# Optimization experiments

Hardware: AMD Instinct MI355X
Metric: run time of the kernel (lower is better)

Reference implementation:

```python
import jax, jax.numpy as jnp
import numpy as np

D_MODEL = 1024
D_STATE = 16
D_CONV = 4
EXPAND = 2
INNER = EXPAND * D_MODEL          # 2048
DT_RANK = max(D_MODEL // 16, 1)   # 64
B_SZ, L_SEQ = 2, 2048


def setup_inputs() -> dict:
    key = jax.random.key(0)
    ks = jax.random.split(key, 9)
    s = 0.02
    x = jax.random.normal(ks[0], (B_SZ, L_SEQ, D_MODEL), jnp.float32)
    W_in = jax.random.normal(ks[1], (2 * INNER, D_MODEL), jnp.float32) * s
    conv_w = jax.random.normal(ks[2], (INNER, 1, D_CONV), jnp.float32) * s
    conv_b = jax.random.normal(ks[3], (INNER,), jnp.float32) * s
    W_x = jax.random.normal(ks[4], (DT_RANK + 2 * D_STATE, INNER), jnp.float32) * s
    W_dt = jax.random.normal(ks[5], (INNER, DT_RANK), jnp.float32) * s
    b_dt = jax.random.normal(ks[6], (INNER,), jnp.float32) * s
    A_log = jnp.log(jnp.broadcast_to(
        jnp.arange(1, D_STATE + 1, dtype=jnp.float32), (INNER, D_STATE)))
    D_param = jnp.ones((INNER,), jnp.float32)
    W_out = jax.random.normal(ks[7], (D_MODEL, INNER), jnp.float32) * s
    return {"x": x, "W_in": W_in, "conv_w": conv_w, "conv_b": conv_b,
            "W_x": W_x, "W_dt": W_dt, "b_dt": b_dt,
            "A_log": A_log, "D_param": D_param, "W_out": W_out}


def _mamba_fwd(x, W_in, conv_w, conv_b, W_x, W_dt, b_dt, A_log, D_param, W_out):
    b, l, d = x.shape
    inner = W_in.shape[0] // 2
    dt_rank = W_dt.shape[1]
    n = A_log.shape[1]

    # in_proj and chunk
    xr = x @ W_in.T                               # [B, L, 2*inner]
    xs, res = xr[..., :inner], xr[..., inner:]

    # depthwise causal conv1d (torch pads d_conv-1 both sides then truncates to l,
    # equivalent to left-pad d_conv-1 + valid conv)
    xc = jnp.transpose(xs, (0, 2, 1))             # [B, inner, L]
    xc = jax.lax.conv_general_dilated(
        xc, conv_w, window_strides=(1,),
        padding=[(conv_w.shape[-1] - 1, 0)],
        dimension_numbers=("NCH", "OIH", "NCH"),
        feature_group_count=inner) + conv_b[None, :, None]
    xs = jax.nn.silu(jnp.transpose(xc, (0, 2, 1)))  # [B, L, inner]

    # x_proj -> dt, B, C
    x_dbl = xs @ W_x.T                            # [B, L, dt_rank + 2n]
    dt = jax.nn.softplus(x_dbl[..., :dt_rank] @ W_dt.T + b_dt)  # [B, L, inner]
    Bm = x_dbl[..., dt_rank:dt_rank + n]          # [B, L, n]
    Cm = x_dbl[..., dt_rank + n:]                 # [B, L, n]

    A = -jnp.exp(A_log)                           # [inner, n]
    # NOTE: original applies softplus a second time inside selective_scan
    dt2 = jax.nn.softplus(dt)

    def step(h, inp):
        dt_t, B_t, C_t, x_t = inp                 # [B,inner],[B,n],[B,n],[B,inner]
        dA = jnp.exp(dt_t[..., None] * A)         # [B, inner, n]
        h = dA * h + dt_t[..., None] * B_t[:, None, :] * x_t[..., None]
        y = jnp.einsum("bdn,bn->bd", h, C_t)
        return h, y

    tfirst = lambda a: jnp.swapaxes(a, 0, 1)      # [B,L,...] -> [L,B,...]
    h0 = jnp.zeros((b, inner, n), x.dtype)
    _, ys = jax.lax.scan(step, h0, (tfirst(dt2), tfirst(Bm), tfirst(Cm), tfirst(xs)))
    y = jnp.swapaxes(ys, 0, 1)                    # [B, L, inner]

    y = y + xs * D_param
    y = y * jax.nn.silu(res)
    return y @ W_out.T                            # [B, L, d_model]


def reference(x, W_in, conv_w, conv_b, W_x, W_dt, b_dt, A_log, D_param, W_out):
    return _mamba_fwd(x, W_in, conv_w, conv_b, W_x, W_dt, b_dt, A_log, D_param, W_out)
```

## Files before the change

kernel.cpp:

```cpp
#include <hip/hip_runtime.h>

#define LSEQ 2048

typedef unsigned short u16;
typedef short short8 __attribute__((ext_vector_type(8)));
typedef float f32x4 __attribute__((ext_vector_type(4)));

__device__ __forceinline__ u16 f2bf(float f) {
    unsigned u = __builtin_bit_cast(unsigned, f);
    u += 0x7fffu + ((u >> 16) & 1u);
    return (u16)(u >> 16);
}
__device__ __forceinline__ float bf2f(u16 h) {
    return __builtin_bit_cast(float, (unsigned)h << 16);
}
__device__ __forceinline__ float softplus_f(float x) {
    return fmaxf(x, 0.f) + __logf(1.f + __expf(-fabsf(x)));
}
__device__ __forceinline__ float silu_f(float x) {
    return x / (1.f + __expf(-x));
}

__device__ __forceinline__ void epowers(float e1, float* ep) {
    float e2 = e1 * e1, e4 = e2 * e2, e8 = e4 * e4;
    ep[0] = e1;       ep[1] = e2;       ep[2] = e1 * e2;  ep[3] = e4;
    ep[4] = e1 * e4;  ep[5] = e2 * e4;  ep[6] = ep[2] * e4; ep[7] = e8;
    ep[8] = e1 * e8;  ep[9] = e2 * e8;  ep[10] = ep[2] * e8; ep[11] = e4 * e8;
    ep[12] = ep[4] * e8; ep[13] = ep[5] * e8; ep[14] = ep[6] * e8; ep[15] = e8 * e8;
}

__device__ __forceinline__ void gl16(const u16* g, u16* l) {
    __builtin_amdgcn_global_load_lds(
        (const __attribute__((address_space(1))) unsigned int*)g,
        (__attribute__((address_space(3))) unsigned int*)l, 16, 0, 0);
}

#define BAR()   asm volatile("s_barrier" ::: "memory")
#define MEMFENCE() do { asm volatile("" ::: "memory"); __builtin_amdgcn_sched_barrier(0); } while (0)

template <int MODE>
__global__ __launch_bounds__(512, 2) void gemm8p(
    const u16* __restrict__ A, int lda,
    const u16* __restrict__ W, int ldw,
    float* __restrict__ C, int ldc, size_t zstride,
    int K, int n_store, u16* __restrict__ out2, u16* __restrict__ out2b)
{
    extern __shared__ u16 lds[];
    const int t    = threadIdx.x;
    const int lane = t & 63, quad = lane >> 4, lr = lane & 15;
    const int w    = t >> 6;
    const int wr   = w >> 2, wc = w & 3;

    int bm, bn;
    if (MODE == 3) {
        int lin = blockIdx.y * 16 + blockIdx.x;
        int swz = (lin & 7) * 32 + (lin >> 3);
        bm = swz >> 4; bn = swz & 15;
    } else {
        bm = blockIdx.y; bn = blockIdx.x;
    }
    const int z  = blockIdx.z;
    const int kz = z * K;

    const int srow = t >> 3;
    const int scol = (((t & 7) ^ (srow & 7)) << 3);
    const u16* pAg = A + (size_t)(bm * 256 + srow) * lda + kz + scol;
    const u16* pWg = W + (size_t)(bn * 256 + srow) * ldw + kz + scol;
    const int ldsw = w * 512;

#define STA(buf, h, i, k0) \
    gl16(pAg + (size_t)((h) * 128 + (i) * 64) * lda + (k0), \
         lds + (buf) * 32768 + (h) * 8192 + (i) * 4096 + ldsw)
#define STB(buf, h, i, k0) \
    gl16(pWg + (size_t)((h) * 128 + (i) * 64) * ldw + (k0), \
         lds + (buf) * 32768 + 16384 + (h) * 8192 + (i) * 4096 + ldsw)

    const int aBase = (wr * 128 + lr) * 64;
    const int bBase = 16384 + (wc * 64 + lr) * 64;
    const int cof0  = ((quad)     ^ (lr & 7)) << 3;
    const int cof1  = ((quad | 4) ^ (lr & 7)) << 3;

    f32x4 acc[8][4];
    #pragma unroll
    for (int i = 0; i < 8; ++i)
        #pragma unroll
        for (int j = 0; j < 4; ++j)
            acc[i][j] = (f32x4){0.f, 0.f, 0.f, 0.f};

    short8 aL[4][2], aH[4][2], bL[2][2], bH[2][2];

    const int NK = K >> 6;
    STA(0,0,0,0); STA(0,0,1,0); STA(0,1,0,0); STA(0,1,1,0);
    STB(0,0,0,0); STB(0,0,1,0); STB(0,1,0,0); STB(0,1,1,0);
    if (NK > 1) {
        STA(1,0,0,64); STA(1,0,1,64); STA(1,1,0,64); STA(1,1,1,64);
        asm volatile("s_waitcnt vmcnt(4)" ::: "memory");
    } else {
        asm volatile("s_waitcnt vmcnt(0)" ::: "memory");
    }
    BAR();

    int cur = 0;
    for (int tt = 0; tt < NK; ++tt) {
        const int nxt = cur ^ 1;
        const u16* Lb = lds + cur * 32768;
        const int k1 = (tt + 1) << 6, k2 = (tt + 2) << 6;
        const bool s1 = (tt + 1) < NK, s2 = (tt + 2) < NK;

        #pragma unroll
        for (int mi = 0; mi < 4; ++mi) {
            aL[mi][0] = *(const short8*)&Lb[aBase + mi * 1024 + cof0];
            aL[mi][1] = *(const short8*)&Lb[aBase + mi * 1024 + cof1];
        }
        #pragma unroll
        for (int ni = 0; ni < 2; ++ni) {
            bL[ni][0] = *(const short8*)&Lb[bBase + ni * 1024 + cof0];
            bL[ni][1] = *(const short8*)&Lb[bBase + ni * 1024 + cof1];
        }
        MEMFENCE();
        #pragma unroll
        for (int ni = 0; ni < 2; ++ni) {
            bH[ni][0] = *(const short8*)&Lb[bBase + (ni + 2) * 1024 + cof0];
            bH[ni][1] = *(const short8*)&Lb[bBase + (ni + 2) * 1024 + cof1];
        }
        MEMFENCE();
        #pragma unroll
        for (int mi = 0; mi < 4; ++mi) {
            aH[mi][0] = *(const short8*)&Lb[aBase + (mi + 4) * 1024 + cof0];
            aH[mi][1] = *(const short8*)&Lb[aBase + (mi + 4) * 1024 + cof1];
        }
        MEMFENCE();

        if (s1) { STB(nxt, 0, 0, k1); STB(nxt, 0, 1, k1); }
        asm volatile("s_waitcnt lgkmcnt(12)" ::: "memory");
        __builtin_amdgcn_sched_barrier(0);
        __builtin_amdgcn_s_setprio(1);
        #pragma unroll
        for (int mi = 0; mi < 4; ++mi)
            #pragma unroll
            for (int ni = 0; ni < 2; ++ni) {
                acc[mi][ni] = __builtin_amdgcn_mfma_f32_16x16x32_bf16(aL[mi][0], bL[ni][0], acc[mi][ni], 0, 0, 0);
                acc[mi][ni] = __builtin_amdgcn_mfma_f32_16x16x32_bf16(aL[mi][1], bL[ni][1], acc[mi][ni], 0, 0, 0);
            }
        __builtin_amdgcn_s_setprio(0);

        if (s1) { STB(nxt, 1, 0, k1); STB(nxt, 1, 1, k1); }
        asm volatile("s_waitcnt lgkmcnt(8)" ::: "memory");
        __builtin_amdgcn_sched_barrier(0);
        __builtin_amdgcn_s_setprio(1);
        #pragma unroll
        for (int mi = 0; mi < 4; ++mi)
            #pragma unroll
            for (int ni = 0; ni < 2; ++ni) {
                acc[mi][ni + 2] = __builtin_amdgcn_mfma_f32_16x16x32_bf16(aL[mi][0], bH[ni][0], acc[mi][ni + 2], 0, 0, 0);
                acc[mi][ni + 2] = __builtin_amdgcn_mfma_f32_16x16x32_bf16(aL[mi][1], bH[ni][1], acc[mi][ni + 2], 0, 0, 0);
            }
        __builtin_amdgcn_s_setprio(0);

        asm volatile("s_waitcnt lgkmcnt(0)" ::: "memory");
        __builtin_amdgcn_sched_barrier(0);
        __builtin_amdgcn_s_setprio(1);
        #pragma unroll
        for (int mi = 0; mi < 4; ++mi)
            #pragma unroll
            for (int ni = 0; ni < 2; ++ni) {
                acc[mi + 4][ni + 2] = __builtin_amdgcn_mfma_f32_16x16x32_bf16(aH[mi][0], bH[ni][0], acc[mi + 4][ni + 2], 0, 0, 0);
                acc[mi + 4][ni + 2] = __builtin_amdgcn_mfma_f32_16x16x32_bf16(aH[mi][1], bH[ni][1], acc[mi + 4][ni + 2], 0, 0, 0);
            }
        __builtin_amdgcn_s_setprio(0);
        BAR();

        if (s2) { STA(cur, 0, 0, k2); STA(cur, 0, 1, k2);
                  STA(cur, 1, 0, k2); STA(cur, 1, 1, k2); }
        __builtin_amdgcn_s_setprio(1);
        #pragma unroll
        for (int mi = 0; mi < 4; ++mi)
            #pragma unroll
            for (int ni = 0; ni < 2; ++ni) {
                acc[mi + 4][ni] = __builtin_amdgcn_mfma_f32_16x16x32_bf16(aH[mi][0], bL[ni][0], acc[mi + 4][ni], 0, 0, 0);
                acc[mi + 4][ni] = __builtin_amdgcn_mfma_f32_16x16x32_bf16(aH[mi][1], bL[ni][1], acc[mi + 4][ni], 0, 0, 0);
            }
        __builtin_amdgcn_s_setprio(0);
        if (s2)      asm volatile("s_waitcnt vmcnt(4)" ::: "memory");
        else if (s1) asm volatile("s_waitcnt vmcnt(0)" ::: "memory");
        BAR();
        cur = nxt;
    }
#undef STA
#undef STB

    #pragma unroll
    for (int mi = 0; mi < 8; ++mi) {
        #pragma unroll
        for (int ni = 0; ni < 4; ++ni) {
            const int col = bn * 256 + wc * 64 + ni * 16 + lr;
            #pragma unroll
            for (int p = 0; p < 4; ++p) {
                const int row = bm * 256 + wr * 128 + mi * 16 + quad * 4 + p;
                float v = acc[mi][ni][p];
                if (MODE == 0) {
                    if (col < n_store)
                        C[(size_t)z * zstride + (size_t)row * ldc + col] = v;
                } else {
                    if (col < 2048) out2 [(size_t)row * 2048 + col] = f2bf(v);
                    else            out2b[(size_t)row * 2048 + col - 2048] = f2bf(silu_f(v));
                }
            }
        }
    }
}

template <int MODE>
__global__ __launch_bounds__(256, 2) void gemm128(
    const u16* __restrict__ A, int lda,
    const u16* __restrict__ W, int ldw,
    float* __restrict__ C, int ldc,
    int K, int n_store, u16* __restrict__ out2, u16* __restrict__ out2b)
{
    extern __shared__ u16 lds[];
    const int t    = threadIdx.x;
    const int lane = t & 63, quad = lane >> 4, lr = lane & 15;
    const int w    = t >> 6;
    const int wr   = w >> 1, wc = w & 1;

    const int nbx = gridDim.x;
    const int nwg = nbx * gridDim.y;
    int lin = blockIdx.y * nbx + blockIdx.x;
    int q8  = nwg >> 3;
    int swz = (lin & 7) * q8 + (lin >> 3);
    const int bm = swz / nbx, bn = swz % nbx;

    const int srow = t >> 3;
    const int scol = (((t & 7) ^ (srow & 7)) << 3);
    const u16* pAg = A + (size_t)(bm * 128 + srow) * lda + scol;
    const u16* pWg = W + (size_t)(bn * 128 + srow) * ldw + scol;
    const int ldsw = w * 512;

#define STA(buf, i, k0) \
    gl16(pAg + (size_t)((i) * 32) * lda + (k0), \
         lds + (buf) * 16384 + (i) * 2048 + ldsw)
#define STB(buf, i, k0) \
    gl16(pWg + (size_t)((i) * 32) * ldw + (k0), \
         lds + (buf) * 16384 + 8192 + (i) * 2048 + ldsw)

    const int aBase = (wr * 64 + lr) * 64;
    const int bBase = 8192 + (wc * 64 + lr) * 64;
    const int cof0  = ((quad)     ^ (lr & 7)) << 3;
    const int cof1  = ((quad | 4) ^ (lr & 7)) << 3;

    f32x4 acc[4][4];
    #pragma unroll
    for (int i = 0; i < 4; ++i)
        #pragma unroll
        for (int j = 0; j < 4; ++j)
            acc[i][j] = (f32x4){0.f, 0.f, 0.f, 0.f};

    short8 aL[2][2], aH[2][2], bL[2][2], bH[2][2];

    const int NK = K >> 6;
    STA(0,0,0); STA(0,1,0); STA(0,2,0); STA(0,3,0);
    STB(0,0,0); STB(0,1,0); STB(0,2,0); STB(0,3,0);
    if (NK > 1) {
        STA(1,0,64); STA(1,1,64); STA(1,2,64); STA(1,3,64);
        asm volatile("s_waitcnt vmcnt(4)" ::: "memory");
    } else {
        asm volatile("s_waitcnt vmcnt(0)" ::: "memory");
    }
    BAR();

    int cur = 0;
    for (int tt = 0; tt < NK; ++tt) {
        const int nxt = cur ^ 1;
        const u16* Lb = lds + cur * 16384;
        const int k1 = (tt + 1) << 6, k2 = (tt + 2) << 6;
        const bool s1 = (tt + 1) < NK, s2 = (tt + 2) < NK;

        #pragma unroll
        for (int mi = 0; mi < 2; ++mi) {
            aL[mi][0] = *(const short8*)&Lb[aBase + mi * 1024 + cof0];
            aL[mi][1] = *(const short8*)&Lb[aBase + mi * 1024 + cof1];
        }
        #pragma unroll
        for (int ni = 0; ni < 2; ++ni) {
            bL[ni][0] = *(const short8*)&Lb[bBase + ni * 1024 + cof0];
            bL[ni][1] = *(const short8*)&Lb[bBase + ni * 1024 + cof1];
        }
        MEMFENCE();
        #pragma unroll
        for (int ni = 0; ni < 2; ++ni) {
            bH[ni][0] = *(const short8*)&Lb[bBase + (ni + 2) * 1024 + cof0];
            bH[ni][1] = *(const short8*)&Lb[bBase + (ni + 2) * 1024 + cof1];
        }
        MEMFENCE();
        #pragma unroll
        for (int mi = 0; mi < 2; ++mi) {
            aH[mi][0] = *(const short8*)&Lb[aBase + (mi + 2) * 1024 + cof0];
            aH[mi][1] = *(const short8*)&Lb[aBase + (mi + 2) * 1024 + cof1];
        }
        MEMFENCE();

        if (s1) { STB(nxt, 0, k1); STB(nxt, 1, k1); }
        asm volatile("s_waitcnt lgkmcnt(8)" ::: "memory");
        __builtin_amdgcn_sched_barrier(0);
        __builtin_amdgcn_s_setprio(1);
        #pragma unroll
        for (int mi = 0; mi < 2; ++mi)
            #pragma unroll
            for (int ni = 0; ni < 2; ++ni) {
                acc[mi][ni] = __builtin_amdgcn_mfma_f32_16x16x32_bf16(aL[mi][0], bL[ni][0], acc[mi][ni], 0, 0, 0);
                acc[mi][ni] = __builtin_amdgcn_mfma_f32_16x16x32_bf16(aL[mi][1], bL[ni][1], acc[mi][ni], 0, 0, 0);
            }
        __builtin_amdgcn_s_setprio(0);

        if (s1) { STB(nxt, 2, k1); STB(nxt, 3, k1); }
        asm volatile("s_waitcnt lgkmcnt(4)" ::: "memory");
        __builtin_amdgcn_sched_barrier(0);
        __builtin_amdgcn_s_setprio(1);
        #pragma unroll
        for (int mi = 0; mi < 2; ++mi)
            #pragma unroll
            for (int ni = 0; ni < 2; ++ni) {
                acc[mi][ni + 2] = __builtin_amdgcn_mfma_f32_16x16x32_bf16(aL[mi][0], bH[ni][0], acc[mi][ni + 2], 0, 0, 0);
                acc[mi][ni + 2] = __builtin_amdgcn_mfma_f32_16x16x32_bf16(aL[mi][1], bH[ni][1], acc[mi][ni + 2], 0, 0, 0);
            }
        __builtin_amdgcn_s_setprio(0);

        asm volatile("s_waitcnt lgkmcnt(0)" ::: "memory");
        __builtin_amdgcn_sched_barrier(0);
        __builtin_amdgcn_s_setprio(1);
        #pragma unroll
        for (int mi = 0; mi < 2; ++mi)
            #pragma unroll
            for (int ni = 0; ni < 2; ++ni) {
                acc[mi + 2][ni + 2] = __builtin_amdgcn_mfma_f32_16x16x32_bf16(aH[mi][0], bH[ni][0], acc[mi + 2][ni + 2], 0, 0, 0);
                acc[mi + 2][ni + 2] = __builtin_amdgcn_mfma_f32_16x16x32_bf16(aH[mi][1], bH[ni][1], acc[mi + 2][ni + 2], 0, 0, 0);
            }
        __builtin_amdgcn_s_setprio(0);
        BAR();

        if (s2) { STA(cur, 0, k2); STA(cur, 1, k2);
                  STA(cur, 2, k2); STA(cur, 3, k2); }
        __builtin_amdgcn_s_setprio(1);
        #pragma unroll
        for (int mi = 0; mi < 2; ++mi)
            #pragma unroll
            for (int ni = 0; ni < 2; ++ni) {
                acc[mi + 2][ni] = __builtin_amdgcn_mfma_f32_16x16x32_bf16(aH[mi][0], bL[ni][0], acc[mi + 2][ni], 0, 0, 0);
                acc[mi + 2][ni] = __builtin_amdgcn_mfma_f32_16x16x32_bf16(aH[mi][1], bL[ni][1], acc[mi + 2][ni], 0, 0, 0);
            }
        __builtin_amdgcn_s_setprio(0);
        if (s2)      asm volatile("s_waitcnt vmcnt(4)" ::: "memory");
        else if (s1) asm volatile("s_waitcnt vmcnt(0)" ::: "memory");
        BAR();
        cur = nxt;
    }
#undef STA
#undef STB

    #pragma unroll
    for (int mi = 0; mi < 4; ++mi) {
        #pragma unroll
        for (int ni = 0; ni < 4; ++ni) {
            const int col = bn * 128 + wc * 64 + ni * 16 + lr;
            #pragma unroll
            for (int p = 0; p < 4; ++p) {
                const int row = bm * 128 + wr * 64 + mi * 16 + quad * 4 + p;
                float v = acc[mi][ni][p];
                if (MODE == 0) {
                    if (col < n_store) C[(size_t)row * ldc + col] = v;
                } else {
                    if (col < 2048) out2 [(size_t)row * 2048 + col] = f2bf(v);
                    else            out2b[(size_t)row * 2048 + col - 2048] = f2bf(silu_f(v));
                }
            }
        }
    }
}

template <int MODE>
__global__ __launch_bounds__(256, 1) void gemm_bf16(
    const u16* __restrict__ A, int lda,
    const u16* __restrict__ W, int ldw,
    float* __restrict__ C, int ldc,
    int kslice, const float* __restrict__ bias,
    int n_store, u16* __restrict__ out2, u16* __restrict__ out2b)
{
    __shared__ u16 As[2 * 128 * 32];
    __shared__ u16 Ws[2 * 128 * 32];
    const int t    = threadIdx.x;
    const int bm   = blockIdx.y, bn = blockIdx.x, bz = blockIdx.z;
    const int lane = t & 63, quad = lane >> 4, lr = lane & 15;
    const int wv   = t >> 6;
    const int wm   = (wv >> 1) * 64, wn = (wv & 1) * 64;
    const int gr2  = lane >> 2;
    const int gc2  = (lane & 3) * 8;

    const u16* Ab = A + (size_t)(bm * 128) * lda + (size_t)bz * kslice;
    const u16* Wb = W + (size_t)(bn * 128) * ldw + (size_t)bz * kslice;

    f32x4 acc[4][4];
    #pragma unroll
    for (int i = 0; i < 4; ++i)
        #pragma unroll
        for (int j = 0; j < 4; ++j)
            acc[i][j] = (f32x4){0.f, 0.f, 0.f, 0.f};

    const int nk = kslice >> 6;
    for (int kb = 0; kb < nk; ++kb) {
        const int k0 = kb << 6;
        #pragma unroll
        for (int q = 0; q < 4; ++q) {
            const int e  = wv * 4 + q;
            const int rg = e >> 1, pn = e & 1;
            gl16(Ab + (size_t)(rg * 16 + gr2) * lda + k0 + pn * 32 + gc2,
                 &As[pn * 4096 + rg * 512]);
            gl16(Wb + (size_t)(rg * 16 + gr2) * ldw + k0 + pn * 32 + gc2,
                 &Ws[pn * 4096 + rg * 512]);
        }
        __syncthreads();
        #pragma unroll
        for (int st = 0; st < 2; ++st) {
            short8 af[4], bfr[4];
            #pragma unroll
            for (int mi = 0; mi < 4; ++mi)
                af[mi] = *(const short8*)&As[st * 4096 + (wm + mi * 16 + lr) * 32 + quad * 8];
            #pragma unroll
            for (int ni = 0; ni < 4; ++ni)
                bfr[ni] = *(const short8*)&Ws[st * 4096 + (wn + ni * 16 + lr) * 32 + quad * 8];
            #pragma unroll
            for (int mi = 0; mi < 4; ++mi)
                #pragma unroll
                for (int ni = 0; ni < 4; ++ni)
                    acc[mi][ni] = __builtin_amdgcn_mfma_f32_16x16x32_bf16(af[mi], bfr[ni], acc[mi][ni], 0, 0, 0);
        }
        __syncthreads();
    }

    #pragma unroll
    for (int mi = 0; mi < 4; ++mi) {
        #pragma unroll
        for (int ni = 0; ni < 4; ++ni) {
            int col = bn * 128 + wn + ni * 16 + lr;
            #pragma unroll
            for (int p = 0; p < 4; ++p) {
                int row = bm * 128 + wm + mi * 16 + quad * 4 + p;
                float v = acc[mi][ni][p];
                if (MODE == 0) {
                    if (col < n_store) C[(size_t)row * ldc + col] = v;
                } else if (MODE == 2) {
                    atomicAdd(&C[(size_t)row * ldc + col], v);
                } else if (MODE == 4) {
                    if (col < n_store)
                        C[(size_t)bz * 524288 + (size_t)row * ldc + col] = v;
                } else {
                    if (col < 2048) out2 [(size_t)row * 2048 + col] = f2bf(v);
                    else            out2b[(size_t)row * 2048 + col - 2048] = f2bf(silu_f(v));
                }
            }
        }
    }
}

__global__ __launch_bounds__(256) void reduce8_k(
    const float* __restrict__ P, float* __restrict__ xdbl)
{
    size_t i = ((size_t)blockIdx.x * 256 + threadIdx.x) * 4;
    float4 s = *(const float4*)(P + i);
    #pragma unroll
    for (int z = 1; z < 8; ++z) {
        float4 v = *(const float4*)(P + (size_t)z * 524288 + i);
        s.x += v.x; s.y += v.y; s.z += v.z; s.w += v.w;
    }
    *(float4*)(xdbl + i) = s;
}

__global__ __launch_bounds__(256, 1) void gemm_dt(
    const float* __restrict__ A128,
    const u16*  __restrict__ Wdt,
    const float* __restrict__ bias,
    u16* __restrict__ dtb)
{
    const int t    = threadIdx.x;
    const int bn   = blockIdx.x, bm = blockIdx.y;
    const int lane = t & 63, quad = lane >> 4, lr = lane & 15;
    const int wv   = t >> 6;
    const int wm   = (wv >> 1) * 64, wn = (wv & 1) * 64;

    f32x4 acc[4][4];
    #pragma unroll
    for (int i = 0; i < 4; ++i)
        #pragma unroll
        for (int j = 0; j < 4; ++j)
            acc[i][j] = (f32x4){0.f, 0.f, 0.f, 0.f};

    #pragma unroll
    for (int st = 0; st < 2; ++st) {
        short8 af[4], bfr[4];
        #pragma unroll
        for (int mi = 0; mi < 4; ++mi) {
            int row = bm * 128 + wm + mi * 16 + lr;
            const float* ap = A128 + (size_t)row * 128 + st * 32 + quad * 8;
            float4 a0 = *(const float4*)ap;
            float4 a1 = *(const float4*)(ap + 4);
            short8 v;
            v[0] = (short)f2bf(a0.x); v[1] = (short)f2bf(a0.y);
            v[2] = (short)f2bf(a0.z); v[3] = (short)f2bf(a0.w);
            v[4] = (short)f2bf(a1.x); v[5] = (short)f2bf(a1.y);
            v[6] = (short)f2bf(a1.z); v[7] = (short)f2bf(a1.w);
            af[mi] = v;
        }
        #pragma unroll
        for (int ni = 0; ni < 4; ++ni) {
            int n = bn * 128 + wn + ni * 16 + lr;
            bfr[ni] = *(const short8*)(Wdt + (size_t)n * 64 + st * 32 + quad * 8);
        }
        #pragma unroll
        for (int mi = 0; mi < 4; ++mi)
            #pragma unroll
            for (int ni = 0; ni < 4; ++ni)
                acc[mi][ni] = __builtin_amdgcn_mfma_f32_16x16x32_bf16(af[mi], bfr[ni], acc[mi][ni], 0, 0, 0);
    }

    #pragma unroll
    for (int mi = 0; mi < 4; ++mi) {
        #pragma unroll
        for (int ni = 0; ni < 4; ++ni) {
            int col = bn * 128 + wn + ni * 16 + lr;
            #pragma unroll
            for (int p = 0; p < 4; ++p) {
                int row = bm * 128 + wm + mi * 16 + quad * 4 + p;
                float v = softplus_f(softplus_f(acc[mi][ni][p] + bias[col]));
                dtb[(size_t)row * 2048 + col] = f2bf(v);
            }
        }
    }
}

__device__ __forceinline__ void cast4(const float* __restrict__ s, u16* __restrict__ d, int i) {
    float4 v = *(const float4*)(s + (size_t)i * 4);
    ushort4 o;
    o.x = f2bf(v.x); o.y = f2bf(v.y); o.z = f2bf(v.z); o.w = f2bf(v.w);
    *(ushort4*)(d + (size_t)i * 4) = o;
}
__global__ __launch_bounds__(256) void k_prep(
    const float* __restrict__ x, const float* __restrict__ W_in,
    const float* __restrict__ W_out, const float* __restrict__ W_dt,
    const float* __restrict__ W_x,
    u16* __restrict__ xb, u16* __restrict__ winb, u16* __restrict__ woutb,
    u16* __restrict__ wdtb, u16* __restrict__ wxpb)
{
    int i = blockIdx.x * 256 + threadIdx.x;
    if (i < 1048576) { cast4(x, xb, i); return; }
    i -= 1048576;
    if (i < 1048576) { cast4(W_in, winb, i); return; }
    i -= 1048576;
    if (i < 524288)  { cast4(W_out, woutb, i); return; }
    i -= 524288;
    if (i < 32768)   { cast4(W_dt, wdtb, i); return; }
    i -= 32768;
    {
        int i4 = i * 4;
        int row = i4 >> 11;
        ushort4 o;
        if (row < 96) {
            float4 v = *(const float4*)(W_x + i4);
            o.x = f2bf(v.x); o.y = f2bf(v.y); o.z = f2bf(v.z); o.w = f2bf(v.w);
        } else { o.x = o.y = o.z = o.w = 0; }
        *(ushort4*)(wxpb + i4) = o;
    }
}

__global__ __launch_bounds__(256) void conv_silu_k(
    const u16* __restrict__ xrb, const float* __restrict__ cw,
    const float* __restrict__ cb, u16* __restrict__ xsb)
{
    int i = blockIdx.x * 256 + threadIdx.x;
    int i4 = i * 4;
    int d = i4 & 2047;
    int t = (i4 >> 11) & 2047;
    int b = i4 >> 22;
    const u16* base = xrb + ((size_t)b * LSEQ) * 2048 + d;
    float4 acc = *(const float4*)(cb + d);
    float4 w0 = *(const float4*)(cw + d * 4);
    float4 w1 = *(const float4*)(cw + d * 4 + 4);
    float4 w2 = *(const float4*)(cw + d * 4 + 8);
    float4 w3 = *(const float4*)(cw + d * 4 + 12);
    {
        ushort4 u = *(const ushort4*)(base + (size_t)t * 2048);
        acc.x += w0.w * bf2f(u.x); acc.y += w1.w * bf2f(u.y);
        acc.z += w2.w * bf2f(u.z); acc.w += w3.w * bf2f(u.w);
    }
    if (t >= 1) {
        ushort4 u = *(const ushort4*)(base + (size_t)(t - 1) * 2048);
        acc.x += w0.z * bf2f(u.x); acc.y += w1.z * bf2f(u.y);
        acc.z += w2.z * bf2f(u.z); acc.w += w3.z * bf2f(u.w);
    }
    if (t >= 2) {
        ushort4 u = *(const ushort4*)(base + (size_t)(t - 2) * 2048);
        acc.x += w0.y * bf2f(u.x); acc.y += w1.y * bf2f(u.y);
        acc.z += w2.y * bf2f(u.z); acc.w += w3.y * bf2f(u.w);
    }
    if (t >= 3) {
        ushort4 u = *(const ushort4*)(base + (size_t)(t - 3) * 2048);
        acc.x += w0.x * bf2f(u.x); acc.y += w1.x * bf2f(u.y);
        acc.z += w2.x * bf2f(u.z); acc.w += w3.x * bf2f(u.w);
    }
    ushort4 o;
    o.x = f2bf(silu_f(acc.x)); o.y = f2bf(silu_f(acc.y));
    o.z = f2bf(silu_f(acc.z)); o.w = f2bf(silu_f(acc.w));
    *(ushort4*)(xsb + i4) = o;
}

__global__ __launch_bounds__(256) void scan_p1(
    const u16*  __restrict__ dtb,
    const u16*  __restrict__ xsb,
    const float* __restrict__ xdw,
    float* __restrict__ csP, float* __restrict__ csS)
{
    const int tid = threadIdx.x;
    const int d  = blockIdx.x * 256 + tid;
    const int ch = blockIdx.y;
    const int b  = blockIdx.z;
    const int r0 = b * LSEQ + ch * 64;
    __shared__ float sB[64 * 16];
    for (int i = tid; i < 1024; i += 256) {
        int tt = i >> 4, n = i & 15;
        sB[i] = xdw[(size_t)(r0 + tt) * 128 + 64 + n];
    }
    __syncthreads();
    float h[16];
    #pragma unroll
    for (int n = 0; n < 16; ++n) h[n] = 0.f;
    const u16* dp = dtb + (size_t)r0 * 2048 + d;
    const u16* xp = xsb + (size_t)r0 * 2048 + d;
    float sdt = 0.f;
    for (int tb = 0; tb < 64; tb += 8) {
        float dt8[8], x8[8];
        #pragma unroll
        for (int j = 0; j < 8; ++j) {
            dt8[j] = bf2f(dp[(size_t)(tb + j) * 2048]);
            x8[j]  = bf2f(xp[(size_t)(tb + j) * 2048]);
        }
        #pragma unroll
        for (int j = 0; j < 8; ++j) {
            const int tt = tb + j;
            float dtv = dt8[j];
            float dx = dtv * x8[j];
            sdt += dtv;
            float ep[16];
            epowers(__expf(-dtv), ep);
            #pragma unroll
            for (int n = 0; n < 16; ++n)
                h[n] = ep[n] * h[n] + dx * sB[tt * 16 + n];
        }
    }
    size_t o = ((size_t)b * 32 + ch) * 32768 + (size_t)d * 16;
    float ep[16];
    epowers(__expf(-sdt), ep);
    #pragma unroll
    for (int q = 0; q < 4; ++q) {
        f32x4 P, S;
        #pragma unroll
        for (int j = 0; j < 4; ++j) { P[j] = ep[q * 4 + j]; S[j] = h[q * 4 + j]; }
        *(f32x4*)(csP + o + q * 4) = P;
        *(f32x4*)(csS + o + q * 4) = S;
    }
}

__global__ __launch_bounds__(256) void scan_p2(
    const float* __restrict__ csP, float* __restrict__ csS)
{
    int i = blockIdx.x * 256 + threadIdx.x;
    int b = i >> 15;
    int j = i & 32767;
    float h = 0.f;
    size_t base = (size_t)b * 32 * 32768 + j;
    for (int ch = 0; ch < 32; ch += 4) {
        size_t o0 = base + (size_t)(ch + 0) * 32768;
        size_t o1 = base + (size_t)(ch + 1) * 32768;
        size_t o2 = base + (size_t)(ch + 2) * 32768;
        size_t o3 = base + (size_t)(ch + 3) * 32768;
        float p0 = csP[o0], s0 = csS[o0];
        float p1 = csP[o1], s1 = csS[o1];
        float p2 = csP[o2], s2 = csS[o2];
        float p3 = csP[o3], s3 = csS[o3];
        csS[o0] = h; h = p0 * h + s0;
        csS[o1] = h; h = p1 * h + s1;
        csS[o2] = h; h = p2 * h + s2;
        csS[o3] = h; h = p3 * h + s3;
    }
}

__global__ __launch_bounds__(256) void scan_p3(
    const u16*  __restrict__ dtb,
    const u16*  __restrict__ resb,
    const u16*  __restrict__ xsb,
    const float* __restrict__ xdw,
    const float* __restrict__ Dp,
    const float* __restrict__ hin,
    u16* __restrict__ yab)
{
    const int tid = threadIdx.x;
    const int d  = blockIdx.x * 256 + tid;
    const int ch = blockIdx.y;
    const int b  = blockIdx.z;
    const int r0 = b * LSEQ + ch * 64;
    __shared__ float sBC[64 * 32];
    for (int i = tid; i < 2048; i += 256) {
        int tt = i >> 5, c = i & 31;
        sBC[i] = xdw[(size_t)(r0 + tt) * 128 + 64 + c];
    }
    __syncthreads();
    float h[16];
    size_t o = ((size_t)b * 32 + ch) * 32768 + (size_t)d * 16;
    #pragma unroll
    for (int q = 0; q < 4; ++q) {
        f32x4 hv = *(const f32x4*)(hin + o + q * 4);
        h[q * 4 + 0] = hv[0]; h[q * 4 + 1] = hv[1];
        h[q * 4 + 2] = hv[2]; h[q * 4 + 3] = hv[3];
    }
    const float Dv = Dp[d];
    const u16* dp = dtb  + (size_t)r0 * 2048 + d;
    const u16* rp = resb + (size_t)r0 * 2048 + d;
    const u16* xp = xsb  + (size_t)r0 * 2048 + d;
    u16* yp = yab + (size_t)r0 * 2048 + d;
    for (int tb = 0; tb < 64; tb += 8) {
        float dt8[8], r8[8], x8[8];
        #pragma unroll
        for (int j = 0; j < 8; ++j) {
            dt8[j] = bf2f(dp[(size_t)(tb + j) * 2048]);
            r8[j]  = bf2f(rp[(size_t)(tb + j) * 2048]);
            x8[j]  = bf2f(xp[(size_t)(tb + j) * 2048]);
        }
        #pragma unroll
        for (int j = 0; j < 8; ++j) {
            const int tt = tb + j;
            float dtv = dt8[j];
            float xv  = x8[j];
            float dx = dtv * xv;
            float ep[16];
            epowers(__expf(-dtv), ep);
            #pragma unroll
            for (int n = 0; n < 16; ++n)
                h[n] = ep[n] * h[n] + dx * sBC[tt * 32 + n];
            float yq[8];
            #pragma unroll
            for (int n = 0; n < 8; ++n)
                yq[n] = h[2 * n] * sBC[tt * 32 + 16 + 2 * n]
                      + h[2 * n + 1] * sBC[tt * 32 + 16 + 2 * n + 1];
            float y = ((yq[0] + yq[1]) + (yq[2] + yq[3]))
                    + ((yq[4] + yq[5]) + (yq[6] + yq[7]));
            yp[(size_t)tt * 2048] = f2bf((y + xv * Dv) * r8[j]);
        }
    }
}

extern "C" void kernel_launch(void* const* d_in, const int* in_sizes, int n_in,
                              void* d_out, int out_size, void* d_ws, size_t ws_size,
                              hipStream_t stream)
{
    const float* x     = (const float*)d_in[0];
    const float* W_in  = (const float*)d_in[1];
    const float* cw    = (const float*)d_in[2];
    const float* cb    = (const float*)d_in[3];
    const float* W_x   = (const float*)d_in[4];
    const float* W_dt  = (const float*)d_in[5];
    const float* b_dt  = (const float*)d_in[6];
    const float* Dp    = (const float*)d_in[8];
    const float* W_out = (const float*)d_in[9];
    float* out = (float*)d_out;

    float* ws = (float*)d_ws;
    u16*  xrb       = (u16*)(ws);
    u16*  resb      = (u16*)(ws +  4194304);
    u16*  xsb       = (u16*)(ws +  8388608);
    u16*  dtb       = (u16*)(ws + 12582912);
    u16*  yab       = (u16*)(ws + 16777216);
    float* csS      = ws + 21364736;
    u16*  woutb     = (u16*)(ws + 25559040);
    u16*  wxpb      = (u16*)(ws + 26607616);
    u16*  wdtb      = (u16*)(ws + 26738688);
    float* xdbl128f = ws + 27066368;
    float* gpart3 = ws;
    float* csP    = ws;
    u16*  xb   = (u16*)(ws + 21364736);
    u16*  winb = (u16*)(ws + 23461888);

    static bool s_attr = false;
    if (!s_attr) {
        hipFuncSetAttribute(reinterpret_cast<const void*>(&gemm8p<3>),
                            hipFuncAttributeMaxDynamicSharedMemorySize, 131072);
        hipFuncSetAttribute(reinterpret_cast<const void*>(&gemm128<0>),
                            hipFuncAttributeMaxDynamicSharedMemorySize, 65536);
        s_attr = true;
    }

    dim3 blk(256);
    k_prep<<<dim3(10624), blk, 0, stream>>>(x, W_in, W_out, W_dt, W_x,
                                            xb, winb, woutb, wdtb, wxpb);
    gemm8p<3><<<dim3(16, 16, 1), dim3(512), 131072, stream>>>(
        xb, 1024, winb, 1024, nullptr, 0, 0, 1024, 4096, xrb, resb);
    conv_silu_k<<<dim3(8192), blk, 0, stream>>>(xrb, cw, cb, xsb);
    gemm_bf16<4><<<dim3(1, 32, 8), blk, 0, stream>>>(xsb, 2048, wxpb, 2048, gpart3, 128, 256, nullptr, 128, nullptr, nullptr);
    reduce8_k<<<dim3(512), blk, 0, stream>>>(gpart3, xdbl128f);
    gemm_dt<<<dim3(16, 32), blk, 0, stream>>>(xdbl128f, wdtb, b_dt, dtb);
    scan_p1<<<dim3(8, 32, 2), blk, 0, stream>>>(dtb, xsb, xdbl128f, csP, csS);
    scan_p2<<<dim3(256), blk, 0, stream>>>(csP, csS);
    scan_p3<<<dim3(8, 32, 2), blk, 0, stream>>>(dtb, resb, xsb, xdbl128f, Dp, csS, yab);
    gemm128<0><<<dim3(8, 32), dim3(256), 65536, stream>>>(
        yab, 2048, woutb, 2048, out, 1024, 2048, 1024, nullptr, nullptr);
}
```

Baseline: 323.1 us.

## Stage scan inputs through double-buffered LDS with 16-byte vector loads

The scan_p1 and scan_p3 kernels now load dt, xs and res tiles of 16 timesteps by 256 channels using 16-byte vector loads into double-buffered shared memory. Each group's global loads are issued before the previous group is computed, so they overlap. scan_p3 also stages its bf16 outputs in shared memory and writes them back as vectorized rows. This replaces per-thread strided 2-byte global accesses, which were poorly vectorized. The cost is extra LDS use, which may lower occupancy, plus extra barriers per group.

```diff
diff --git a/kernel.cpp b/kernel.cpp
--- a/kernel.cpp
+++ b/kernel.cpp
@@ -618,45 +618,76 @@
     float* __restrict__ csP, float* __restrict__ csS)
 {
     const int tid = threadIdx.x;
-    const int d  = blockIdx.x * 256 + tid;
-    const int ch = blockIdx.y;
-    const int b  = blockIdx.z;
-    const int r0 = b * LSEQ + ch * 64;
+    const int d0  = blockIdx.x * 256;
+    const int d   = d0 + tid;
+    const int ch  = blockIdx.y;
+    const int b   = blockIdx.z;
+    const int r0  = b * LSEQ + ch * 64;
     __shared__ float sB[64 * 16];
+    __shared__ u16 sdt[2][16 * 256];
+    __shared__ u16 sx [2][16 * 256];
     for (int i = tid; i < 1024; i += 256) {
         int tt = i >> 4, n = i & 15;
         sB[i] = xdw[(size_t)(r0 + tt) * 128 + 64 + n];
     }
+    const int lr_ = tid >> 5;
+    const int lc_ = (tid & 31) * 8;
+
+    short8 ld_d0, ld_d1, ld_x0, ld_x1;
+#define LOADG1(g) do { \
+    ld_d0 = *(const short8*)(dtb + (size_t)(r0 + (g) * 16 + lr_) * 2048 + d0 + lc_); \
+    ld_d1 = *(const short8*)(dtb + (size_t)(r0 + (g) * 16 + 8 + lr_) * 2048 + d0 + lc_); \
+    ld_x0 = *(const short8*)(xsb + (size_t)(r0 + (g) * 16 + lr_) * 2048 + d0 + lc_); \
+    ld_x1 = *(const short8*)(xsb + (size_t)(r0 + (g) * 16 + 8 + lr_) * 2048 + d0 + lc_); \
+} while (0)
+#define WRITEG1(buf) do { \
+    *(short8*)&sdt[buf][lr_ * 256 + lc_]       = ld_d0; \
+    *(short8*)&sdt[buf][(8 + lr_) * 256 + lc_] = ld_d1; \
+    *(short8*)&sx [buf][lr_ * 256 + lc_]       = ld_x0; \
+    *(short8*)&sx [buf][(8 + lr_) * 256 + lc_] = ld_x1; \
+} while (0)
+
+    LOADG1(0); WRITEG1(0);
     __syncthreads();
+
     float h[16];
     #pragma unroll
     for (int n = 0; n < 16; ++n) h[n] = 0.f;
-    const u16* dp = dtb + (size_t)r0 * 2048 + d;
-    const u16* xp = xsb + (size_t)r0 * 2048 + d;
-    float sdt = 0.f;
-    for (int tb = 0; tb < 64; tb += 8) {
-        float dt8[8], x8[8];
-        #pragma unroll
-        for (int j = 0; j < 8; ++j) {
-            dt8[j] = bf2f(dp[(size_t)(tb + j) * 2048]);
-            x8[j]  = bf2f(xp[(size_t)(tb + j) * 2048]);
-        }
-        #pragma unroll
-        for (int j = 0; j < 8; ++j) {
-            const int tt = tb + j;
-            float dtv = dt8[j];
-            float dx = dtv * x8[j];
-            sdt += dtv;
-            float ep[16];
-            epowers(__expf(-dtv), ep);
-            #pragma unroll
-            for (int n = 0; n < 16; ++n)
-                h[n] = ep[n] * h[n] + dx * sB[tt * 16 + n];
-        }
-    }
+    float sdtacc = 0.f;
+
+    for (int g = 0; g < 4; ++g) {
+        const int pb = g & 1;
+        if (g < 3) LOADG1(g + 1);
+        #pragma unroll
+        for (int tb = 0; tb < 16; tb += 8) {
+            float dt8[8], x8[8];
+            #pragma unroll
+            for (int j = 0; j < 8; ++j) {
+                dt8[j] = bf2f(sdt[pb][(tb + j) * 256 + tid]);
+                x8[j]  = bf2f(sx [pb][(tb + j) * 256 + tid]);
+            }
+            #pragma unroll
+            for (int j = 0; j < 8; ++j) {
+                const int tt = g * 16 + tb + j;
+                float dtv = dt8[j];
+                float dx = dtv * x8[j];
+                sdtacc += dtv;
+                float ep[16];
+                epowers(__expf(-dtv), ep);
+                #pragma unroll
+                for (int n = 0; n < 16; ++n)
+                    h[n] = ep[n] * h[n] + dx * sB[tt * 16 + n];
+            }
+        }
+        if (g < 3) WRITEG1(pb ^ 1);
+        __syncthreads();
+    }
+#undef LOADG1
+#undef WRITEG1
+
     size_t o = ((size_t)b * 32 + ch) * 32768 + (size_t)d * 16;
     float ep[16];
-    epowers(__expf(-sdt), ep);
+    epowers(__expf(-sdtacc), ep);
     #pragma unroll
     for (int q = 0; q < 4; ++q) {
         f32x4 P, S;
@@ -701,16 +732,44 @@
     u16* __restrict__ yab)
 {
     const int tid = threadIdx.x;
-    const int d  = blockIdx.x * 256 + tid;
-    const int ch = blockIdx.y;
-    const int b  = blockIdx.z;
-    const int r0 = b * LSEQ + ch * 64;
+    const int d0  = blockIdx.x * 256;
+    const int d   = d0 + tid;
+    const int ch  = blockIdx.y;
+    const int b   = blockIdx.z;
+    const int r0  = b * LSEQ + ch * 64;
     __shared__ float sBC[64 * 32];
+    __shared__ u16 sdt[2][16 * 256];
+    __shared__ u16 sx [2][16 * 256];
+    __shared__ u16 sr [2][16 * 256];
+    __shared__ u16 sy [16 * 256];
     for (int i = tid; i < 2048; i += 256) {
         int tt = i >> 5, c = i & 31;
         sBC[i] = xdw[(size_t)(r0 + tt) * 128 + 64 + c];
     }
+    const int lr_ = tid >> 5;
+    const int lc_ = (tid & 31) * 8;
+
+    short8 ld_d0, ld_d1, ld_x0, ld_x1, ld_r0, ld_r1;
+#define LOADG3(g) do { \
+    ld_d0 = *(const short8*)(dtb  + (size_t)(r0 + (g) * 16 + lr_) * 2048 + d0 + lc_); \
+    ld_d1 = *(const short8*)(dtb  + (size_t)(r0 + (g) * 16 + 8 + lr_) * 2048 + d0 + lc_); \
+    ld_x0 = *(const short8*)(xsb  + (size_t)(r0 + (g) * 16 + lr_) * 2048 + d0 + lc_); \
+    ld_x1 = *(const short8*)(xsb  + (size_t)(r0 + (g) * 16 + 8 + lr_) * 2048 + d0 + lc_); \
+    ld_r0 = *(const short8*)(resb + (size_t)(r0 + (g) * 16 + lr_) * 2048 + d0 + lc_); \
+    ld_r1 = *(const short8*)(resb + (size_t)(r0 + (g) * 16 + 8 + lr_) * 2048 + d0 + lc_); \
+} while (0)
+#define WRITEG3(buf) do { \
+    *(short8*)&sdt[buf][lr_ * 256 + lc_]       = ld_d0; \
+    *(short8*)&sdt[buf][(8 + lr_) * 256 + lc_] = ld_d1; \
+    *(short8*)&sx [buf][lr_ * 256 + lc_]       = ld_x0; \
+    *(short8*)&sx [buf][(8 + lr_) * 256 + lc_] = ld_x1; \
+    *(short8*)&sr [buf][lr_ * 256 + lc_]       = ld_r0; \
+    *(short8*)&sr [buf][(8 + lr_) * 256 + lc_] = ld_r1; \
+} while (0)
+
+    LOADG3(0); WRITEG3(0);
     __syncthreads();
+
     float h[16];
     size_t o = ((size_t)b * 32 + ch) * 32768 + (size_t)d * 16;
     #pragma unroll
@@ -720,39 +779,52 @@
         h[q * 4 + 2] = hv[2]; h[q * 4 + 3] = hv[3];
     }
     const float Dv = Dp[d];
-    const u16* dp = dtb  + (size_t)r0 * 2048 + d;
-    const u16* rp = resb + (size_t)r0 * 2048 + d;
-    const u16* xp = xsb  + (size_t)r0 * 2048 + d;
-    u16* yp = yab + (size_t)r0 * 2048 + d;
-    for (int tb = 0; tb < 64; tb += 8) {
-        float dt8[8], r8[8], x8[8];
-        #pragma unroll
-        for (int j = 0; j < 8; ++j) {
-            dt8[j] = bf2f(dp[(size_t)(tb + j) * 2048]);
-            r8[j]  = bf2f(rp[(size_t)(tb + j) * 2048]);
-            x8[j]  = bf2f(xp[(size_t)(tb + j) * 2048]);
-        }
-        #pragma unroll
-        for (int j = 0; j < 8; ++j) {
-            const int tt = tb + j;
-            float dtv = dt8[j];
-            float xv  = x8[j];
-            float dx = dtv * xv;
-            float ep[16];
-            epowers(__expf(-dtv), ep);
-            #pragma unroll
-            for (int n = 0; n < 16; ++n)
-                h[n] = ep[n] * h[n] + dx * sBC[tt * 32 + n];
-            float yq[8];
-            #pragma unroll
-            for (int n = 0; n < 8; ++n)
-                yq[n] = h[2 * n] * sBC[tt * 32 + 16 + 2 * n]
-                      + h[2 * n + 1] * sBC[tt * 32 + 16 + 2 * n + 1];
-            float y = ((yq[0] + yq[1]) + (yq[2] + yq[3]))
-                    + ((yq[4] + yq[5]) + (yq[6] + yq[7]));
-            yp[(size_t)tt * 2048] = f2bf((y + xv * Dv) * r8[j]);
-        }
-    }
+
+    for (int g = 0; g < 4; ++g) {
+        const int pb = g & 1;
+        if (g < 3) LOADG3(g + 1);
+        #pragma unroll
+        for (int tb = 0; tb < 16; tb += 8) {
+            float dt8[8], r8[8], x8[8];
+            #pragma unroll
+            for (int j = 0; j < 8; ++j) {
+                dt8[j] = bf2f(sdt[pb][(tb + j) * 256 + tid]);
+                r8[j]  = bf2f(sr [pb][(tb + j) * 256 + tid]);
+                x8[j]  = bf2f(sx [pb][(tb + j) * 256 + tid]);
+            }
+            #pragma unroll
+            for (int j = 0; j < 8; ++j) {
+                const int tt = g * 16 + tb + j;
+                float dtv = dt8[j];
+                float xv  = x8[j];
+                float dx = dtv * xv;
+                float ep[16];
+                epowers(__expf(-dtv), ep);
+                #pragma unroll
+                for (int n = 0; n < 16; ++n)
+                    h[n] = ep[n] * h[n] + dx * sBC[tt * 32 + n];
+                float yq[8];
+                #pragma unroll
+                for (int n = 0; n < 8; ++n)
+                    yq[n] = h[2 * n] * sBC[tt * 32 + 16 + 2 * n]
+                          + h[2 * n + 1] * sBC[tt * 32 + 16 + 2 * n + 1];
+                float y = ((yq[0] + yq[1]) + (yq[2] + yq[3]))
+                        + ((yq[4] + yq[5]) + (yq[6] + yq[7]));
+                sy[(tb + j) * 256 + tid] = f2bf((y + xv * Dv) * r8[j]);
+            }
+        }
+        __syncthreads();
+        {
+            short8 y0 = *(const short8*)&sy[lr_ * 256 + lc_];
+            short8 y1 = *(const short8*)&sy[(8 + lr_) * 256 + lc_];
+            *(short8*)(yab + (size_t)(r0 + g * 16 + lr_) * 2048 + d0 + lc_)     = y0;
+            *(short8*)(yab + (size_t)(r0 + g * 16 + 8 + lr_) * 2048 + d0 + lc_) = y1;
+        }
+        if (g < 3) WRITEG3(pb ^ 1);
+        __syncthreads();
+    }
+#undef LOADG3
+#undef WRITEG3
 }
 
 extern "C" void kernel_launch(void* const* d_in, const int* in_sizes, int n_in,
```

Result: faster. 310.0 us (-4.0%).
